# Kernel tuning notes

Measured on AMD Instinct MI355X. Metric: run time of the kernel, lower is better.

## Reference

```python
import jax, jax.numpy as jnp
import numpy as np

N_EMBD = 2048
HEAD_SIZE = 128

def setup_inputs() -> dict:
    key = jax.random.key(0)
    kx, kk, kq, kv = jax.random.split(key, 4)
    bound = 1.0 / np.sqrt(N_EMBD)  # torch Linear default init range
    x = jax.random.normal(kx, (4, 4096, N_EMBD), dtype=jnp.float32)
    Wk = jax.random.uniform(kk, (N_EMBD, HEAD_SIZE), jnp.float32, -bound, bound)
    Wq = jax.random.uniform(kq, (N_EMBD, HEAD_SIZE), jnp.float32, -bound, bound)
    Wv = jax.random.uniform(kv, (N_EMBD, HEAD_SIZE), jnp.float32, -bound, bound)
    return {"x": x, "Wk": Wk, "Wq": Wq, "Wv": Wv}

def reference(x, Wk, Wq, Wv):
    B, T, C = x.shape
    k = jnp.einsum('btc,ch->bth', x, Wk)
    q = jnp.einsum('btc,ch->bth', x, Wq)
    v = jnp.einsum('btc,ch->bth', x, Wv)
    # NOTE: original scales by C**-0.5 where C = n_embd (input dim), not head_size
    scores = jnp.einsum('bth,bsh->bts', q, k) * (C ** -0.5)
    causal = jnp.tril(jnp.ones((T, T), dtype=bool))  # [T,T]
    scores = jnp.where(causal, scores, -jnp.inf)
    probs = jax.nn.softmax(scores, axis=-1)
    # dropout_probability = 0.0 -> identity
    return jnp.einsum('bts,bsh->bth', probs, v)
```

## Files before the change

### kernel.cpp

```cpp
#include <hip/hip_runtime.h>
#include <hip/hip_bf16.h>

#define T_SEQ 4096
#define NB 4
#define CEMB 2048
#define HS 128

typedef __attribute__((ext_vector_type(8))) short bf16x8;
typedef __attribute__((ext_vector_type(4))) float f32x4;
typedef __attribute__((ext_vector_type(16))) float f32x16;

__device__ inline short f2bf(float f) {
    union { float f; unsigned u; } v; v.f = f;
    unsigned r = v.u + 0x7FFFu + ((v.u >> 16) & 1u);
    return (short)(r >> 16);
}

__device__ inline unsigned pk2(float lo, float hi) {
    unsigned r;
    asm("v_cvt_pk_bf16_f32 %0, %1, %2" : "=v"(r) : "v"(lo), "v"(hi));
    return r;
}

__device__ inline void gld16(const void* gsrc, void* lds) {
    __builtin_amdgcn_global_load_lds(
        (const __attribute__((address_space(1))) unsigned*)gsrc,
        (__attribute__((address_space(3))) unsigned*)lds, 16, 0, 0);
}

__global__ __launch_bounds__(256) void wt_kernel(
    const float* __restrict__ Wq, const float* __restrict__ Wk,
    const float* __restrict__ Wv, short* __restrict__ Wt) {
    int d = blockIdx.x * 256 + threadIdx.x;
    int mat = d >> 18;
    int rm  = d & 262143;
    int s   = rm >> 13;
    int e   = rm & 8191;
    int p   = e * 2;
    int n   = p >> 7;
    int lin = p ^ ((n & 7) << 4);
    int kk  = (lin & 127) >> 1;
    int k   = s * 64 + kk;
    const float* W = (mat == 0) ? Wq : (mat == 1) ? Wk : Wv;
    Wt[d] = f2bf(W[k * HS + n]);
}

__global__ __launch_bounds__(256, 3) void proj_kernel(
    const float* __restrict__ x, const short* __restrict__ Wt,
    short* __restrict__ qg, short* __restrict__ kg, short* __restrict__ vtg) {
    __shared__ short Wlds[3][8192];

    const int tid = threadIdx.x;
    const int w   = tid >> 6;
    const int l   = tid & 63;
    const int lg  = l >> 4;
    const int lr  = l & 15;

    const int bid = blockIdx.x;
    const int wk  = (bid & 7) * 96 + (bid >> 3);
    const int mat = wk % 3;
    const int m0  = (wk / 3) * 64;

    const short* Wp = Wt + (long)mat * 262144;

    f32x4 acc[8];
    #pragma unroll
    for (int b = 0; b < 8; b++) acc[b] = (f32x4){0.f, 0.f, 0.f, 0.f};

    const float* xrow = x + (long)(m0 + w * 16 + lr) * CEMB;
    const int sw = (lr & 7) << 4;

    float4 xs[3][4];

#define STAGE(S, B) do {                                                   \
        const short* gp_ = Wp + (long)(S) * 8192 + (long)(w * 4) * 512 + l * 8; \
        gld16(gp_,        &Wlds[B][(w * 4 + 0) * 512]);                    \
        gld16(gp_ + 512,  &Wlds[B][(w * 4 + 1) * 512]);                    \
        gld16(gp_ + 1024, &Wlds[B][(w * 4 + 2) * 512]);                    \
        gld16(gp_ + 1536, &Wlds[B][(w * 4 + 3) * 512]);                    \
    } while (0)

#define LOADX(S, B) do {                                                   \
        const float* xn_ = xrow + (S) * 64;                                \
        xs[B][0] = *reinterpret_cast<const float4*>(xn_ + lg * 8);         \
        xs[B][1] = *reinterpret_cast<const float4*>(xn_ + lg * 8 + 4);     \
        xs[B][2] = *reinterpret_cast<const float4*>(xn_ + 32 + lg * 8);    \
        xs[B][3] = *reinterpret_cast<const float4*>(xn_ + 32 + lg * 8 + 4);\
    } while (0)

    STAGE(0, 0);
    LOADX(0, 0);
    STAGE(1, 1);
    LOADX(1, 1);

#define STEP(S, B0, B2) do {                                               \
        asm volatile("s_waitcnt vmcnt(8) lgkmcnt(0)\n\ts_barrier" ::: "memory"); \
        if ((S) + 2 < 32) { STAGE((S) + 2, B2); LOADX((S) + 2, B2); }      \
        bf16x8 a0, a1;                                                     \
        a0[0] = f2bf(xs[B0][0].x); a0[1] = f2bf(xs[B0][0].y);              \
        a0[2] = f2bf(xs[B0][0].z); a0[3] = f2bf(xs[B0][0].w);              \
        a0[4] = f2bf(xs[B0][1].x); a0[5] = f2bf(xs[B0][1].y);              \
        a0[6] = f2bf(xs[B0][1].z); a0[7] = f2bf(xs[B0][1].w);              \
        a1[0] = f2bf(xs[B0][2].x); a1[1] = f2bf(xs[B0][2].y);              \
        a1[2] = f2bf(xs[B0][2].z); a1[3] = f2bf(xs[B0][2].w);              \
        a1[4] = f2bf(xs[B0][3].x); a1[5] = f2bf(xs[B0][3].y);              \
        a1[6] = f2bf(xs[B0][3].z); a1[7] = f2bf(xs[B0][3].w);              \
        const char* lbase_ = (const char*)&Wlds[B0][0];                    \
        _Pragma("unroll")                                                  \
        for (int nt = 0; nt < 8; nt++) {                                   \
            int off_ = (((nt * 16 + lr) * 128 + lg * 16)) ^ sw;            \
            bf16x8 bfr_ = *reinterpret_cast<const bf16x8*>(lbase_ + off_); \
            acc[nt] = __builtin_amdgcn_mfma_f32_16x16x32_bf16(             \
                a0, bfr_, acc[nt], 0, 0, 0);                               \
        }                                                                  \
        _Pragma("unroll")                                                  \
        for (int nt = 0; nt < 8; nt++) {                                   \
            int off_ = (((nt * 16 + lr) * 128 + lg * 16 + 64)) ^ sw;       \
            bf16x8 bfr_ = *reinterpret_cast<const bf16x8*>(lbase_ + off_); \
            acc[nt] = __builtin_amdgcn_mfma_f32_16x16x32_bf16(             \
                a1, bfr_, acc[nt], 0, 0, 0);                               \
        }                                                                  \
    } while (0)

    for (int s = 0; s < 30; s += 3) {
        STEP(s, 0, 2);
        STEP(s + 1, 1, 0);
        STEP(s + 2, 2, 1);
    }
    STEP(30, 0, 2);
    STEP(31, 1, 0);

#undef STEP
#undef LOADX
#undef STAGE

    if (mat == 0) {
        const float scale = 0.0318793851f;
        #pragma unroll
        for (int nt = 0; nt < 8; nt++)
            #pragma unroll
            for (int r = 0; r < 4; r++) {
                int row = m0 + w * 16 + lg * 4 + r;
                qg[(long)row * HS + nt * 16 + lr] = f2bf(acc[nt][r] * scale);
            }
    } else if (mat == 1) {
        short* kt = kg + ((long)(m0 >> 6)) * 8192;
        #pragma unroll
        for (int nt = 0; nt < 8; nt++)
            #pragma unroll
            for (int r = 0; r < 4; r++) {
                int r64  = w * 16 + lg * 4 + r;
                int byte = (r64 * 256 + (nt * 16 + lr) * 2) ^ ((r64 & 7) << 4);
                kt[byte >> 1] = f2bf(acc[nt][r]);
            }
    } else {
        #pragma unroll
        for (int nt = 0; nt < 8; nt++)
            #pragma unroll
            for (int r = 0; r < 4; r++) {
                int row = m0 + w * 16 + lg * 4 + r;
                int b   = row >> 12;
                int tl  = row & 4095;
                vtg[(long)b * (HS * T_SEQ) + (long)(nt * 16 + lr) * T_SEQ + tl]
                    = f2bf(acc[nt][r]);
            }
    }
}

__global__ __launch_bounds__(256, 2) void attn_kernel(
    const short* __restrict__ qg, const short* __restrict__ kg,
    const short* __restrict__ vtg, float* __restrict__ out) {
    __shared__ __align__(16) char pool[65536];
    __shared__ float Lm[4][32];
    __shared__ float Ll[4][32];

    const int tid = threadIdx.x;
    const int w   = tid >> 6;
    const int l   = tid & 63;
    const int c31 = l & 31;
    const int hi  = l >> 5;
    const int hi4 = hi << 2;
    const int hi8 = hi << 3;

    const int bid = blockIdx.x;
    const int xcd = bid & 7;
    const int idx = bid >> 3;
    const int b   = xcd >> 1;
    const int qt  = 127 - ((idx << 1) | (xcd & 1));
    const int q0  = qt * 32;
    const int qrow = q0 + c31;

    const short* kbimg = kg + (long)b * 64 * 8192;
    const short* vb    = vtg + (long)b * HS * T_SEQ;

    short* Kw = (short*)(pool + (w << 14));

#define STAGEK(TILE) do {                                                  \
        const short* gp_ = kbimg + (long)(TILE) * 8192 + l * 8;            \
        _Pragma("unroll")                                                  \
        for (int i = 0; i < 16; i++)                                       \
            gld16(gp_ + i * 512, Kw + i * 512 + l * 8);                    \
    } while (0)

    bf16x8 qf[8];
    #pragma unroll
    for (int kc = 0; kc < 8; kc++)
        qf[kc] = *reinterpret_cast<const bf16x8*>(
            &qg[(long)(b * T_SEQ + qrow) * HS + kc * 16 + hi8]);

    f32x16 accO[4];
    #pragma unroll
    for (int nb = 0; nb < 4; nb++)
        #pragma unroll
        for (int i = 0; i < 16; i++) accO[nb][i] = 0.f;
    float mrow = -__builtin_inff();
    float lsum = 0.f;

    const int ntk = (qt >> 1) + 1;

    STAGEK(w);

    const int swz = (c31 & 7) << 4;
    const int rbA = c31 * 256;
    const int rbB = (32 + c31) * 256;

    #pragma unroll 1
    for (int t = w; t < ntk; t += 4) {
        const int kv0 = t * 64;

        asm volatile("s_waitcnt vmcnt(0)" ::: "memory");

        bf16x8 vfA[2][4];
        #pragma unroll
        for (int kc = 0; kc < 2; kc++)
            #pragma unroll
            for (int nb = 0; nb < 4; nb++)
                vfA[kc][nb] = *reinterpret_cast<const bf16x8*>(
                    &vb[(long)(nb * 32 + c31) * T_SEQ + kv0 + kc * 16 + hi8]);

        f32x16 SA, SB;
        #pragma unroll
        for (int i = 0; i < 16; i++) { SA[i] = 0.f; SB[i] = 0.f; }
        __builtin_amdgcn_s_setprio(1);
        #pragma unroll
        for (int kc = 0; kc < 8; kc++) {
            const int cb = kc * 32 + hi * 16;
            bf16x8 ka = *reinterpret_cast<const bf16x8*>(
                (const char*)Kw + ((rbA + cb) ^ swz));
            bf16x8 kb2 = *reinterpret_cast<const bf16x8*>(
                (const char*)Kw + ((rbB + cb) ^ swz));
            SA = __builtin_amdgcn_mfma_f32_32x32x16_bf16(ka,  qf[kc], SA, 0, 0, 0);
            SB = __builtin_amdgcn_mfma_f32_32x32x16_bf16(kb2, qf[kc], SB, 0, 0, 0);
        }
        __builtin_amdgcn_s_setprio(0);

        if (t + 4 < ntk) STAGEK(t + 4);

        float pA[16], pB[16];
        #pragma unroll
        for (int r = 0; r < 16; r++) { pA[r] = SA[r]; pB[r] = SB[r]; }

        if (kv0 + 63 > q0) {
            #pragma unroll
            for (int r = 0; r < 16; r++) {
                int kr = kv0 + (r & 3) + 8 * (r >> 2) + hi4;
                pA[r] = (kr > qrow)      ? -__builtin_inff() : pA[r];
                pB[r] = (kr + 32 > qrow) ? -__builtin_inff() : pB[r];
            }
        }

        float t16[16];
        #pragma unroll
        for (int r = 0; r < 16; r++) t16[r] = fmaxf(pA[r], pB[r]);
        #pragma unroll
        for (int s2 = 8; s2 >= 1; s2 >>= 1)
            #pragma unroll
            for (int r = 0; r < 8; r++)
                if (r < s2) t16[r] = fmaxf(t16[r], t16[r + s2]);
        float mt = fmaxf(t16[0], __shfl_xor(t16[0], 32));

        if (__any(mt > mrow)) {
            float mnew = fmaxf(mrow, mt);
            float fac  = exp2f(mrow - mnew);
            lsum *= fac;
            #pragma unroll
            for (int nb = 0; nb < 4; nb++)
                #pragma unroll
                for (int i = 0; i < 16; i++) accO[nb][i] *= fac;
            mrow = mnew;
        }

        bf16x8 vfB[2][4];
        #pragma unroll
        for (int kc = 0; kc < 2; kc++)
            #pragma unroll
            for (int nb = 0; nb < 4; nb++)
                vfB[kc][nb] = *reinterpret_cast<const bf16x8*>(
                    &vb[(long)(nb * 32 + c31) * T_SEQ + kv0 + (kc + 2) * 16 + hi8]);

        #pragma unroll
        for (int r = 0; r < 16; r++) {
            pA[r] = exp2f(pA[r] - mrow);
            pB[r] = exp2f(pB[r] - mrow);
        }
        float s16[16];
        #pragma unroll
        for (int r = 0; r < 16; r++) s16[r] = pA[r] + pB[r];
        #pragma unroll
        for (int s2 = 8; s2 >= 1; s2 >>= 1)
            #pragma unroll
            for (int r = 0; r < 8; r++)
                if (r < s2) s16[r] += s16[r + s2];
        lsum += s16[0] + __shfl_xor(s16[0], 32);

        bf16x8 pf[4];
        #pragma unroll
        for (int kc = 0; kc < 4; kc++) {
            const int V0 = 2 * kc, V1 = 2 * kc + 1;
            const int r0 = ((V0 >> 2) << 4) | ((V0 & 3) << 2);
            const int r1 = ((V1 >> 2) << 4) | ((V1 & 3) << 2);
#define PSEL(i) ((i) < 16 ? pA[(i) & 15] : pB[(i) & 15])
            unsigned a0 = pk2(PSEL(r0 + 0), PSEL(r0 + 1));
            unsigned a1 = pk2(PSEL(r0 + 2), PSEL(r0 + 3));
            unsigned b0 = pk2(PSEL(r1 + 0), PSEL(r1 + 1));
            unsigned b1 = pk2(PSEL(r1 + 2), PSEL(r1 + 3));
#undef PSEL
            unsigned k0 = hi ? b0 : a0, k1 = hi ? b1 : a1;
            unsigned s0 = hi ? a0 : b0, s1 = hi ? a1 : b1;
            unsigned g0 = (unsigned)__shfl_xor((int)s0, 32);
            unsigned g1 = (unsigned)__shfl_xor((int)s1, 32);
            union { unsigned u[4]; bf16x8 v; } U;
            U.u[0] = hi ? g0 : k0;
            U.u[1] = hi ? g1 : k1;
            U.u[2] = hi ? k0 : g0;
            U.u[3] = hi ? k1 : g1;
            pf[kc] = U.v;
        }

        __builtin_amdgcn_s_setprio(1);
        #pragma unroll
        for (int nb = 0; nb < 4; nb++)
            accO[nb] = __builtin_amdgcn_mfma_f32_32x32x16_bf16(pf[0], vfA[0][nb], accO[nb], 0, 0, 0);
        #pragma unroll
        for (int nb = 0; nb < 4; nb++)
            accO[nb] = __builtin_amdgcn_mfma_f32_32x32x16_bf16(pf[1], vfA[1][nb], accO[nb], 0, 0, 0);
        #pragma unroll
        for (int nb = 0; nb < 4; nb++)
            accO[nb] = __builtin_amdgcn_mfma_f32_32x32x16_bf16(pf[2], vfB[0][nb], accO[nb], 0, 0, 0);
        #pragma unroll
        for (int nb = 0; nb < 4; nb++)
            accO[nb] = __builtin_amdgcn_mfma_f32_32x32x16_bf16(pf[3], vfB[1][nb], accO[nb], 0, 0, 0);
        __builtin_amdgcn_s_setprio(0);
    }
#undef STAGEK

    {
        float* LaccW = (float*)(pool + (w << 14));
        #pragma unroll
        for (int nb = 0; nb < 4; nb++)
            #pragma unroll
            for (int r = 0; r < 16; r++)
                LaccW[((r & 3) + 8 * (r >> 2) + hi4) * 128 + nb * 32 + c31] = accO[nb][r];
        if (l < 32) { Lm[w][c31] = mrow; Ll[w][c31] = lsum; }
    }
    __syncthreads();

    {
        const int row = tid >> 3;
        const int c0  = (tid & 7) * 16;
        float m0 = Lm[0][row], m1 = Lm[1][row], m2 = Lm[2][row], m3 = Lm[3][row];
        float ms = fmaxf(fmaxf(m0, m1), fmaxf(m2, m3));
        float f0 = exp2f(m0 - ms), f1 = exp2f(m1 - ms);
        float f2 = exp2f(m2 - ms), f3 = exp2f(m3 - ms);
        float L = Ll[0][row] * f0 + Ll[1][row] * f1 + Ll[2][row] * f2 + Ll[3][row] * f3;
        float inv = 1.0f / L;
        float* op = &out[((long)b * T_SEQ + q0 + row) * HS + c0];
        const float* L0 = (const float*)(pool);
        const float* L1 = (const float*)(pool + 16384);
        const float* L2 = (const float*)(pool + 32768);
        const float* L3 = (const float*)(pool + 49152);
        #pragma unroll
        for (int j = 0; j < 16; j++) {
            float o = L0[row * 128 + c0 + j] * f0 + L1[row * 128 + c0 + j] * f1
                    + L2[row * 128 + c0 + j] * f2 + L3[row * 128 + c0 + j] * f3;
            op[j] = o * inv;
        }
    }
}

extern "C" void kernel_launch(void* const* d_in, const int* in_sizes, int n_in,
                              void* d_out, int out_size, void* d_ws, size_t ws_size,
                              hipStream_t stream) {
    const float* x  = (const float*)d_in[0];
    const float* Wk = (const float*)d_in[1];
    const float* Wq = (const float*)d_in[2];
    const float* Wv = (const float*)d_in[3];
    float* out = (float*)d_out;

    char* ws = (char*)d_ws;
    short* Wt  = (short*)ws;
    short* qg  = (short*)(ws + 1572864);
    short* kg  = (short*)(ws + 1572864 + 4194304);
    short* vtg = (short*)(ws + 1572864 + 8388608);

    wt_kernel  <<<3072, 256, 0, stream>>>(Wq, Wk, Wv, Wt);
    proj_kernel<<<768,  256, 0, stream>>>(x, Wt, qg, kg, vtg);
    attn_kernel<<<512,  256, 0, stream>>>(qg, kg, vtg, out);
}
```

Baseline: 132.7 us.

## Pair causal query tiles per 8-wave block to balance attention work

The attention kernel now launches 256 blocks of 512 threads (8 waves). Each block handles two 32-row query tiles, qt and 127-qt, one after the other, so every block does about the same amount of causal work. Within each tile the KV tiles are spread across 8 waves instead of 4, and the 8 partial softmax results are merged through 128KB of LDS. The aim is to remove the load imbalance and tail from the triangular causal workload. In exchange there are extra block-wide barriers per phase, and some waves sit idle on short tiles. The larger LDS footprint also allows only one block per CU.

```diff
diff --git a/kernel.cpp b/kernel.cpp
--- a/kernel.cpp
+++ b/kernel.cpp
@@ -167,12 +167,12 @@
     }
 }
 
-__global__ __launch_bounds__(256, 2) void attn_kernel(
+__global__ __launch_bounds__(512, 2) void attn_kernel(
     const short* __restrict__ qg, const short* __restrict__ kg,
     const short* __restrict__ vtg, float* __restrict__ out) {
-    __shared__ __align__(16) char pool[65536];
-    __shared__ float Lm[4][32];
-    __shared__ float Ll[4][32];
+    __shared__ __align__(16) char pool[131072];
+    __shared__ float Lm[8][32];
+    __shared__ float Ll[8][32];
 
     const int tid = threadIdx.x;
     const int w   = tid >> 6;
@@ -186,9 +186,7 @@
     const int xcd = bid & 7;
     const int idx = bid >> 3;
     const int b   = xcd >> 1;
-    const int qt  = 127 - ((idx << 1) | (xcd & 1));
-    const int q0  = qt * 32;
-    const int qrow = q0 + c31;
+    const int qtA = 127 - ((idx << 1) | (xcd & 1));
 
     const short* kbimg = kg + (long)b * 64 * 8192;
     const short* vb    = vtg + (long)b * HS * T_SEQ;
@@ -202,190 +200,201 @@
             gld16(gp_ + i * 512, Kw + i * 512 + l * 8);                    \
     } while (0)
 
-    bf16x8 qf[8];
-    #pragma unroll
-    for (int kc = 0; kc < 8; kc++)
-        qf[kc] = *reinterpret_cast<const bf16x8*>(
-            &qg[(long)(b * T_SEQ + qrow) * HS + kc * 16 + hi8]);
-
-    f32x16 accO[4];
-    #pragma unroll
-    for (int nb = 0; nb < 4; nb++)
-        #pragma unroll
-        for (int i = 0; i < 16; i++) accO[nb][i] = 0.f;
-    float mrow = -__builtin_inff();
-    float lsum = 0.f;
-
-    const int ntk = (qt >> 1) + 1;
-
-    STAGEK(w);
-
     const int swz = (c31 & 7) << 4;
     const int rbA = c31 * 256;
     const int rbB = (32 + c31) * 256;
 
     #pragma unroll 1
-    for (int t = w; t < ntk; t += 4) {
-        const int kv0 = t * 64;
-
-        asm volatile("s_waitcnt vmcnt(0)" ::: "memory");
-
-        bf16x8 vfA[2][4];
+    for (int ph = 0; ph < 2; ++ph) {
+        const int qt   = ph ? (127 - qtA) : qtA;
+        const int q0   = qt * 32;
+        const int qrow = q0 + c31;
+        const int ntk  = (qt >> 1) + 1;
+
+        bf16x8 qf[8];
         #pragma unroll
-        for (int kc = 0; kc < 2; kc++)
-            #pragma unroll
-            for (int nb = 0; nb < 4; nb++)
-                vfA[kc][nb] = *reinterpret_cast<const bf16x8*>(
-                    &vb[(long)(nb * 32 + c31) * T_SEQ + kv0 + kc * 16 + hi8]);
-
-        f32x16 SA, SB;
-        #pragma unroll
-        for (int i = 0; i < 16; i++) { SA[i] = 0.f; SB[i] = 0.f; }
-        __builtin_amdgcn_s_setprio(1);
-        #pragma unroll
-        for (int kc = 0; kc < 8; kc++) {
-            const int cb = kc * 32 + hi * 16;
-            bf16x8 ka = *reinterpret_cast<const bf16x8*>(
-                (const char*)Kw + ((rbA + cb) ^ swz));
-            bf16x8 kb2 = *reinterpret_cast<const bf16x8*>(
-                (const char*)Kw + ((rbB + cb) ^ swz));
-            SA = __builtin_amdgcn_mfma_f32_32x32x16_bf16(ka,  qf[kc], SA, 0, 0, 0);
-            SB = __builtin_amdgcn_mfma_f32_32x32x16_bf16(kb2, qf[kc], SB, 0, 0, 0);
-        }
-        __builtin_amdgcn_s_setprio(0);
-
-        if (t + 4 < ntk) STAGEK(t + 4);
-
-        float pA[16], pB[16];
-        #pragma unroll
-        for (int r = 0; r < 16; r++) { pA[r] = SA[r]; pB[r] = SB[r]; }
-
-        if (kv0 + 63 > q0) {
-            #pragma unroll
-            for (int r = 0; r < 16; r++) {
-                int kr = kv0 + (r & 3) + 8 * (r >> 2) + hi4;
-                pA[r] = (kr > qrow)      ? -__builtin_inff() : pA[r];
-                pB[r] = (kr + 32 > qrow) ? -__builtin_inff() : pB[r];
-            }
-        }
-
-        float t16[16];
-        #pragma unroll
-        for (int r = 0; r < 16; r++) t16[r] = fmaxf(pA[r], pB[r]);
-        #pragma unroll
-        for (int s2 = 8; s2 >= 1; s2 >>= 1)
-            #pragma unroll
-            for (int r = 0; r < 8; r++)
-                if (r < s2) t16[r] = fmaxf(t16[r], t16[r + s2]);
-        float mt = fmaxf(t16[0], __shfl_xor(t16[0], 32));
-
-        if (__any(mt > mrow)) {
-            float mnew = fmaxf(mrow, mt);
-            float fac  = exp2f(mrow - mnew);
-            lsum *= fac;
-            #pragma unroll
-            for (int nb = 0; nb < 4; nb++)
-                #pragma unroll
-                for (int i = 0; i < 16; i++) accO[nb][i] *= fac;
-            mrow = mnew;
-        }
-
-        bf16x8 vfB[2][4];
-        #pragma unroll
-        for (int kc = 0; kc < 2; kc++)
-            #pragma unroll
-            for (int nb = 0; nb < 4; nb++)
-                vfB[kc][nb] = *reinterpret_cast<const bf16x8*>(
-                    &vb[(long)(nb * 32 + c31) * T_SEQ + kv0 + (kc + 2) * 16 + hi8]);
-
-        #pragma unroll
-        for (int r = 0; r < 16; r++) {
-            pA[r] = exp2f(pA[r] - mrow);
-            pB[r] = exp2f(pB[r] - mrow);
-        }
-        float s16[16];
-        #pragma unroll
-        for (int r = 0; r < 16; r++) s16[r] = pA[r] + pB[r];
-        #pragma unroll
-        for (int s2 = 8; s2 >= 1; s2 >>= 1)
-            #pragma unroll
-            for (int r = 0; r < 8; r++)
-                if (r < s2) s16[r] += s16[r + s2];
-        lsum += s16[0] + __shfl_xor(s16[0], 32);
-
-        bf16x8 pf[4];
-        #pragma unroll
-        for (int kc = 0; kc < 4; kc++) {
-            const int V0 = 2 * kc, V1 = 2 * kc + 1;
-            const int r0 = ((V0 >> 2) << 4) | ((V0 & 3) << 2);
-            const int r1 = ((V1 >> 2) << 4) | ((V1 & 3) << 2);
-#define PSEL(i) ((i) < 16 ? pA[(i) & 15] : pB[(i) & 15])
-            unsigned a0 = pk2(PSEL(r0 + 0), PSEL(r0 + 1));
-            unsigned a1 = pk2(PSEL(r0 + 2), PSEL(r0 + 3));
-            unsigned b0 = pk2(PSEL(r1 + 0), PSEL(r1 + 1));
-            unsigned b1 = pk2(PSEL(r1 + 2), PSEL(r1 + 3));
-#undef PSEL
-            unsigned k0 = hi ? b0 : a0, k1 = hi ? b1 : a1;
-            unsigned s0 = hi ? a0 : b0, s1 = hi ? a1 : b1;
-            unsigned g0 = (unsigned)__shfl_xor((int)s0, 32);
-            unsigned g1 = (unsigned)__shfl_xor((int)s1, 32);
-            union { unsigned u[4]; bf16x8 v; } U;
-            U.u[0] = hi ? g0 : k0;
-            U.u[1] = hi ? g1 : k1;
-            U.u[2] = hi ? k0 : g0;
-            U.u[3] = hi ? k1 : g1;
-            pf[kc] = U.v;
-        }
-
-        __builtin_amdgcn_s_setprio(1);
+        for (int kc = 0; kc < 8; kc++)
+            qf[kc] = *reinterpret_cast<const bf16x8*>(
+                &qg[(long)(b * T_SEQ + qrow) * HS + kc * 16 + hi8]);
+
+        f32x16 accO[4];
         #pragma unroll
         for (int nb = 0; nb < 4; nb++)
-            accO[nb] = __builtin_amdgcn_mfma_f32_32x32x16_bf16(pf[0], vfA[0][nb], accO[nb], 0, 0, 0);
-        #pragma unroll
-        for (int nb = 0; nb < 4; nb++)
-            accO[nb] = __builtin_amdgcn_mfma_f32_32x32x16_bf16(pf[1], vfA[1][nb], accO[nb], 0, 0, 0);
-        #pragma unroll
-        for (int nb = 0; nb < 4; nb++)
-            accO[nb] = __builtin_amdgcn_mfma_f32_32x32x16_bf16(pf[2], vfB[0][nb], accO[nb], 0, 0, 0);
-        #pragma unroll
-        for (int nb = 0; nb < 4; nb++)
-            accO[nb] = __builtin_amdgcn_mfma_f32_32x32x16_bf16(pf[3], vfB[1][nb], accO[nb], 0, 0, 0);
-        __builtin_amdgcn_s_setprio(0);
+            #pragma unroll
+            for (int i = 0; i < 16; i++) accO[nb][i] = 0.f;
+        float mrow = -__builtin_inff();
+        float lsum = 0.f;
+
+        if (w < ntk) STAGEK(w);
+
+        #pragma unroll 1
+        for (int t = w; t < ntk; t += 8) {
+            const int kv0 = t * 64;
+
+            asm volatile("s_waitcnt vmcnt(0)" ::: "memory");
+
+            bf16x8 vfA[2][4];
+            #pragma unroll
+            for (int kc = 0; kc < 2; kc++)
+                #pragma unroll
+                for (int nb = 0; nb < 4; nb++)
+                    vfA[kc][nb] = *reinterpret_cast<const bf16x8*>(
+                        &vb[(long)(nb * 32 + c31) * T_SEQ + kv0 + kc * 16 + hi8]);
+
+            f32x16 SA, SB;
+            #pragma unroll
+            for (int i = 0; i < 16; i++) { SA[i] = 0.f; SB[i] = 0.f; }
+            __builtin_amdgcn_s_setprio(1);
+            #pragma unroll
+            for (int kc = 0; kc < 8; kc++) {
+                const int cb = kc * 32 + hi * 16;
+                bf16x8 ka = *reinterpret_cast<const bf16x8*>(
+                    (const char*)Kw + ((rbA + cb) ^ swz));
+                bf16x8 kb2 = *reinterpret_cast<const bf16x8*>(
+                    (const char*)Kw + ((rbB + cb) ^ swz));
+                SA = __builtin_amdgcn_mfma_f32_32x32x16_bf16(ka,  qf[kc], SA, 0, 0, 0);
+                SB = __builtin_amdgcn_mfma_f32_32x32x16_bf16(kb2, qf[kc], SB, 0, 0, 0);
+            }
+            __builtin_amdgcn_s_setprio(0);
+
+            if (t + 8 < ntk) STAGEK(t + 8);
+
+            float pA[16], pB[16];
+            #pragma unroll
+            for (int r = 0; r < 16; r++) { pA[r] = SA[r]; pB[r] = SB[r]; }
+
+            if (kv0 + 63 > q0) {
+                #pragma unroll
+                for (int r = 0; r < 16; r++) {
+                    int kr = kv0 + (r & 3) + 8 * (r >> 2) + hi4;
+                    pA[r] = (kr > qrow)      ? -__builtin_inff() : pA[r];
+                    pB[r] = (kr + 32 > qrow) ? -__builtin_inff() : pB[r];
+                }
+            }
+
+            float t16[16];
+            #pragma unroll
+            for (int r = 0; r < 16; r++) t16[r] = fmaxf(pA[r], pB[r]);
+            #pragma unroll
+            for (int s2 = 8; s2 >= 1; s2 >>= 1)
+                #pragma unroll
+                for (int r = 0; r < 8; r++)
+                    if (r < s2) t16[r] = fmaxf(t16[r], t16[r + s2]);
+            float mt = fmaxf(t16[0], __shfl_xor(t16[0], 32));
+
+            if (__any(mt > mrow)) {
+                float mnew = fmaxf(mrow, mt);
+                float fac  = exp2f(mrow - mnew);
+                lsum *= fac;
+                #pragma unroll
+                for (int nb = 0; nb < 4; nb++)
+                    #pragma unroll
+                    for (int i = 0; i < 16; i++) accO[nb][i] *= fac;
+                mrow = mnew;
+            }
+
+            bf16x8 vfB[2][4];
+            #pragma unroll
+            for (int kc = 0; kc < 2; kc++)
+                #pragma unroll
+                for (int nb = 0; nb < 4; nb++)
+                    vfB[kc][nb] = *reinterpret_cast<const bf16x8*>(
+                        &vb[(long)(nb * 32 + c31) * T_SEQ + kv0 + (kc + 2) * 16 + hi8]);
+
+            #pragma unroll
+            for (int r = 0; r < 16; r++) {
+                pA[r] = exp2f(pA[r] - mrow);
+                pB[r] = exp2f(pB[r] - mrow);
+            }
+            float s16[16];
+            #pragma unroll
+            for (int r = 0; r < 16; r++) s16[r] = pA[r] + pB[r];
+            #pragma unroll
+            for (int s2 = 8; s2 >= 1; s2 >>= 1)
+                #pragma unroll
+                for (int r = 0; r < 8; r++)
+                    if (r < s2) s16[r] += s16[r + s2];
+            lsum += s16[0] + __shfl_xor(s16[0], 32);
+
+            bf16x8 pf[4];
+            #pragma unroll
+            for (int kc = 0; kc < 4; kc++) {
+                const int V0 = 2 * kc, V1 = 2 * kc + 1;
+                const int r0 = ((V0 >> 2) << 4) | ((V0 & 3) << 2);
+                const int r1 = ((V1 >> 2) << 4) | ((V1 & 3) << 2);
+#define PSEL(i) ((i) < 16 ? pA[(i) & 15] : pB[(i) & 15])
+                unsigned a0 = pk2(PSEL(r0 + 0), PSEL(r0 + 1));
+                unsigned a1 = pk2(PSEL(r0 + 2), PSEL(r0 + 3));
+                unsigned b0 = pk2(PSEL(r1 + 0), PSEL(r1 + 1));
+                unsigned b1 = pk2(PSEL(r1 + 2), PSEL(r1 + 3));
+#undef PSEL
+                unsigned k0 = hi ? b0 : a0, k1 = hi ? b1 : a1;
+                unsigned s0 = hi ? a0 : b0, s1 = hi ? a1 : b1;
+                unsigned g0 = (unsigned)__shfl_xor((int)s0, 32);
+                unsigned g1 = (unsigned)__shfl_xor((int)s1, 32);
+                union { unsigned u[4]; bf16x8 v; } U;
+                U.u[0] = hi ? g0 : k0;
+                U.u[1] = hi ? g1 : k1;
+                U.u[2] = hi ? k0 : g0;
+                U.u[3] = hi ? k1 : g1;
+                pf[kc] = U.v;
+            }
+
+            __builtin_amdgcn_s_setprio(1);
+            #pragma unroll
+            for (int nb = 0; nb < 4; nb++)
+                accO[nb] = __builtin_amdgcn_mfma_f32_32x32x16_bf16(pf[0], vfA[0][nb], accO[nb], 0, 0, 0);
+            #pragma unroll
+            for (int nb = 0; nb < 4; nb++)
+                accO[nb] = __builtin_amdgcn_mfma_f32_32x32x16_bf16(pf[1], vfA[1][nb], accO[nb], 0, 0, 0);
+            #pragma unroll
+            for (int nb = 0; nb < 4; nb++)
+                accO[nb] = __builtin_amdgcn_mfma_f32_32x32x16_bf16(pf[2], vfB[0][nb], accO[nb], 0, 0, 0);
+            #pragma unroll
+            for (int nb = 0; nb < 4; nb++)
+                accO[nb] = __builtin_amdgcn_mfma_f32_32x32x16_bf16(pf[3], vfB[1][nb], accO[nb], 0, 0, 0);
+            __builtin_amdgcn_s_setprio(0);
+        }
+
+        __syncthreads();
+        {
+            float* LaccW = (float*)(pool + (w << 14));
+            #pragma unroll
+            for (int nb = 0; nb < 4; nb++)
+                #pragma unroll
+                for (int r = 0; r < 16; r++)
+                    LaccW[((r & 3) + 8 * (r >> 2) + hi4) * 128 + nb * 32 + c31] = accO[nb][r];
+            if (l < 32) { Lm[w][c31] = mrow; Ll[w][c31] = lsum; }
+        }
+        __syncthreads();
+
+        {
+            const int row = tid >> 4;
+            const int c0  = (tid & 15) * 8;
+            float mv[8], lv[8];
+            #pragma unroll
+            for (int p2 = 0; p2 < 8; p2++) { mv[p2] = Lm[p2][row]; lv[p2] = Ll[p2][row]; }
+            float ms = mv[0];
+            #pragma unroll
+            for (int p2 = 1; p2 < 8; p2++) ms = fmaxf(ms, mv[p2]);
+            float fv[8];
+            float L = 0.f;
+            #pragma unroll
+            for (int p2 = 0; p2 < 8; p2++) { fv[p2] = exp2f(mv[p2] - ms); L += lv[p2] * fv[p2]; }
+            float inv = 1.0f / L;
+            float* op = &out[((long)b * T_SEQ + q0 + row) * HS + c0];
+            #pragma unroll
+            for (int j = 0; j < 8; j++) {
+                float o = 0.f;
+                #pragma unroll
+                for (int p2 = 0; p2 < 8; p2++)
+                    o += ((const float*)(pool + (p2 << 14)))[row * 128 + c0 + j] * fv[p2];
+                op[j] = o * inv;
+            }
+        }
+        __syncthreads();
     }
 #undef STAGEK
-
-    {
-        float* LaccW = (float*)(pool + (w << 14));
-        #pragma unroll
-        for (int nb = 0; nb < 4; nb++)
-            #pragma unroll
-            for (int r = 0; r < 16; r++)
-                LaccW[((r & 3) + 8 * (r >> 2) + hi4) * 128 + nb * 32 + c31] = accO[nb][r];
-        if (l < 32) { Lm[w][c31] = mrow; Ll[w][c31] = lsum; }
-    }
-    __syncthreads();
-
-    {
-        const int row = tid >> 3;
-        const int c0  = (tid & 7) * 16;
-        float m0 = Lm[0][row], m1 = Lm[1][row], m2 = Lm[2][row], m3 = Lm[3][row];
-        float ms = fmaxf(fmaxf(m0, m1), fmaxf(m2, m3));
-        float f0 = exp2f(m0 - ms), f1 = exp2f(m1 - ms);
-        float f2 = exp2f(m2 - ms), f3 = exp2f(m3 - ms);
-        float L = Ll[0][row] * f0 + Ll[1][row] * f1 + Ll[2][row] * f2 + Ll[3][row] * f3;
-        float inv = 1.0f / L;
-        float* op = &out[((long)b * T_SEQ + q0 + row) * HS + c0];
-        const float* L0 = (const float*)(pool);
-        const float* L1 = (const float*)(pool + 16384);
-        const float* L2 = (const float*)(pool + 32768);
-        const float* L3 = (const float*)(pool + 49152);
-        #pragma unroll
-        for (int j = 0; j < 16; j++) {
-            float o = L0[row * 128 + c0 + j] * f0 + L1[row * 128 + c0 + j] * f1
-                    + L2[row * 128 + c0 + j] * f2 + L3[row * 128 + c0 + j] * f3;
-            op[j] = o * inv;
-        }
-    }
 }
 
 extern "C" void kernel_launch(void* const* d_in, const int* in_sizes, int n_in,
@@ -405,5 +414,5 @@
 
     wt_kernel  <<<3072, 256, 0, stream>>>(Wq, Wk, Wv, Wt);
     proj_kernel<<<768,  256, 0, stream>>>(x, Wt, qg, kg, vtg);
-    attn_kernel<<<512,  256, 0, stream>>>(qg, kg, vtg, out);
-}
+    attn_kernel<<<256,  512, 0, stream>>>(qg, kg, vtg, out);
+}
```

New measurement: 133.5 us. About the same (+0.5%).
